# Kernel optimization log

Hardware: AMD Instinct MI355X
Metric: run time of the kernel (lower is better)

Reference implementation:

```python
import jax, jax.numpy as jnp
import numpy as np
from jax import lax

DIM = 256
HEADS = 8
EPS = 1e-12  # torch F.normalize default eps
DN = ('NCHW', 'OIHW', 'NCHW')


def conv1x1(x, w):
    return lax.conv_general_dilated(x, w, (1, 1), 'VALID', dimension_numbers=DN)


def dwconv3x3(x, w):
    c = x.shape[1]
    return lax.conv_general_dilated(x, w, (1, 1), ((1, 1), (1, 1)),
                                    dimension_numbers=DN, feature_group_count=c)


def setup_inputs() -> dict:
    key = jax.random.key(0)
    ks = jax.random.split(key, 8)
    B, C, H, W = 4, DIM, 160, 160
    s = lambda fan: 1.0 / np.sqrt(fan)
    return {
        'low': jax.random.normal(ks[0], (B, C, H, W), jnp.float32),
        'high': jax.random.normal(ks[1], (B, C, H, W), jnp.float32),
        'q_w': jax.random.normal(ks[2], (C, C, 1, 1), jnp.float32) * s(C),
        'q_dw_w': jax.random.normal(ks[3], (C, 1, 3, 3), jnp.float32) * s(9),
        'kv_w': jax.random.normal(ks[4], (2 * C, C, 1, 1), jnp.float32) * s(C),
        'kv_dw_w': jax.random.normal(ks[5], (2 * C, 1, 3, 3), jnp.float32) * s(9),
        'proj_w': jax.random.normal(ks[6], (C, C, 1, 1), jnp.float32) * s(C),
        'temperature': jnp.ones((HEADS, 1, 1), jnp.float32),
    }


def reference(low, high, q_w, q_dw_w, kv_w, kv_dw_w, proj_w, temperature):
    B, C, H, W = low.shape
    hw = H * W
    ch = C // HEADS  # channels per head

    q = dwconv3x3(conv1x1(high, q_w), q_dw_w)           # [B, C, H, W]
    kv = dwconv3x3(conv1x1(low, kv_w), kv_dw_w)         # [B, 2C, H, W]
    k, v = jnp.split(kv, 2, axis=1)

    def heads(x):
        return x.reshape(B, HEADS, ch, hw)              # b head c (h w)

    q, k, v = heads(q), heads(k), heads(v)

    # L2-normalize along spatial dim (torch F.normalize semantics)
    q = q / jnp.maximum(jnp.linalg.norm(q, axis=-1, keepdims=True), EPS)
    k = k / jnp.maximum(jnp.linalg.norm(k, axis=-1, keepdims=True), EPS)

    attn = jnp.einsum('bhcn,bhdn->bhcd', q, k) * temperature  # [B, H, ch, ch]
    attn = jax.nn.softmax(attn, axis=-1)
    out = jnp.einsum('bhcd,bhdn->bhcn', attn, v)               # [B, H, ch, hw]

    out = out.reshape(B, C, H, W)
    return conv1x1(out, proj_w)
```

## Files before the change

kernel.cpp:

```cpp
#include <hip/hip_runtime.h>
#include <math.h>

#define HW 25600
#define IMGW 160
#define CDIM 256
#define NB 4
#define NHEADS 8
#define SZB ((long)CDIM * HW)

typedef __attribute__((ext_vector_type(8))) short short8v;
typedef __attribute__((ext_vector_type(4))) float f32x4;
typedef __attribute__((ext_vector_type(8))) unsigned short us8;

union FragU {
    us8 o;
    short8v s;
    unsigned u32[4];
};

__device__ inline unsigned short f2bf(float f) {
    unsigned u = __float_as_uint(f);
    return (unsigned short)((u + 0x7fffu + ((u >> 16) & 1u)) >> 16);
}
__device__ inline float bf2f(unsigned short h) {
    return __uint_as_float(((unsigned)h) << 16);
}

__global__ __launch_bounds__(256) void cvtw_k(
    const float* __restrict__ kv_w, const float* __restrict__ q_w,
    unsigned short* __restrict__ wkv_s, unsigned short* __restrict__ wq_s)
{
    int idx = blockIdx.x * 256 + threadIdx.x;
    int g2 = idx & 3;
    int kt = (idx >> 2) & 7;
    int co = idx >> 5;
    const float* src;
    unsigned short* dst;
    int nco, co_l;
    if (co < 512) { src = kv_w; dst = wkv_s; nco = 512; co_l = co; }
    else          { src = q_w;  dst = wq_s;  nco = 256; co_l = co - 512; }
    src += (long)co_l * CDIM + kt * 32 + g2 * 8;
    us8 v;
#pragma unroll
    for (int u = 0; u < 8; ++u) v[u] = f2bf(src[u]);
    int slot = g2 ^ ((co_l >> 1) & 3);
    *(us8*)(dst + ((long)kt * nco + co_l) * 32 + slot * 8) = v;
}

template<int OUTF32, int XF32>
__global__ __launch_bounds__(256) void gemm3_k(
    const void* __restrict__ Xv, const unsigned short* __restrict__ WS,
    void* __restrict__ outp, long xbs, long wbs, long obs, int nco)
{
    __shared__ __align__(16) char SMEM[36864];
    unsigned short* Wl = (unsigned short*)SMEM;
    unsigned short* Xl = (unsigned short*)(SMEM + 16384);
    const int XST = XF32 ? 5120 : 4096;

    const int t  = threadIdx.x;
    const int l  = t & 63;
    const int wv = t >> 6;
    const int g  = l >> 4;
    const int ln = l & 15;

    const int NX = gridDim.x;
    const int orig = blockIdx.y * NX + blockIdx.x;
    const int chunkp = (NX * gridDim.y) >> 3;
    const int wgid = (orig & 7) * chunkp + (orig >> 3);
    const int co0 = (wgid % NX) * 128;
    const int n0  = (wgid / NX) * 128;

    const long b  = blockIdx.z;
    const unsigned short* Wb  = WS + b * wbs;
    const float* Xfp          = (const float*)Xv + b * xbs;
    const unsigned short* Xbf = (const unsigned short*)Xv + b * xbs;
    const int wr = wv >> 1, wc = wv & 1;

    f32x4 acc[4][4];
#pragma unroll
    for (int i = 0; i < 4; ++i)
#pragma unroll
        for (int j = 0; j < 4; ++j) acc[i][j] = (f32x4){0.f, 0.f, 0.f, 0.f};

    const int lrow = l >> 2;
    const int lgrp = l & 3;
    const int n_l = t & 127;
    const int sb  = (t >> 7) * 2;

    float f[16];

#define STAGE_W(ktv, buf)                                                     \
    {                                                                         \
        _Pragma("unroll")                                                     \
        for (int ii = 0; ii < 2; ++ii) {                                      \
            int instr = wv * 2 + ii;                                          \
            int row = instr * 16 + lrow;                                      \
            const unsigned short* wsrc =                                      \
                Wb + ((long)(ktv) * nco + co0 + row) * 32 + lgrp * 8;         \
            __builtin_amdgcn_global_load_lds(                                 \
                (const __attribute__((address_space(1))) void*)wsrc,          \
                (__attribute__((address_space(3))) void*)                     \
                    &Wl[(buf) * 4096 + instr * 512], 16, 0, 0);               \
        }                                                                     \
    }
#define STAGE_XG(ktv, buf)                                                    \
    {                                                                         \
        _Pragma("unroll")                                                     \
        for (int ii = 0; ii < 2; ++ii) {                                      \
            int instr = wv * 2 + ii;                                          \
            int row = instr * 16 + lrow;                                      \
            const unsigned short* xsrc =                                      \
                Xbf + ((long)(ktv) * HW + n0 + row) * 32 + lgrp * 8;          \
            __builtin_amdgcn_global_load_lds(                                 \
                (const __attribute__((address_space(1))) void*)xsrc,          \
                (__attribute__((address_space(3))) void*)                     \
                    &Xl[(buf) * 4096 + instr * 512], 16, 0, 0);               \
        }                                                                     \
    }
#define LOAD_XF(ktv)                                                          \
    {                                                                         \
        _Pragma("unroll")                                                     \
        for (int si = 0; si < 2; ++si)                                        \
            _Pragma("unroll")                                                 \
            for (int u = 0; u < 8; ++u)                                       \
                f[si * 8 + u] =                                               \
                    Xfp[(long)((ktv) * 32 + (sb + si) * 8 + u) * HW + n0 + n_l]; \
    }
#define WRITE_XF(buf)                                                         \
    {                                                                         \
        _Pragma("unroll")                                                     \
        for (int si = 0; si < 2; ++si) {                                      \
            FragU cv;                                                         \
            _Pragma("unroll")                                                 \
            for (int e2 = 0; e2 < 4; ++e2) {                                  \
                unsigned rr;                                                  \
                asm("v_cvt_pk_bf16_f32 %0, %1, %2"                            \
                    : "=v"(rr) : "v"(f[si * 8 + e2 * 2]),                     \
                      "v"(f[si * 8 + e2 * 2 + 1]));                           \
                cv.u32[e2] = rr;                                              \
            }                                                                 \
            *(us8*)&Xl[(buf) * XST + n_l * 40 + (sb + si) * 8] = cv.o;        \
        }                                                                     \
    }

    STAGE_W(0, 0);
    if (XF32) { LOAD_XF(0); WRITE_XF(0); }
    else      { STAGE_XG(0, 0); }
    __syncthreads();

    for (int kt = 0; kt < 8; ++kt) {
        const int cur = kt & 1, nxt = cur ^ 1;
        if (kt < 7) {
            STAGE_W(kt + 1, nxt);
            if (XF32) { LOAD_XF(kt + 1); }
            else      { STAGE_XG(kt + 1, nxt); }
        }
        FragU A_[4], B_[4];
#pragma unroll
        for (int i = 0; i < 4; ++i) {
            int row = wr * 64 + i * 16 + ln;
            int slot = g ^ ((row >> 1) & 3);
            A_[i].o = *(const us8*)&Wl[cur * 4096 + row * 32 + slot * 8];
        }
        if (XF32) {
#pragma unroll
            for (int j = 0; j < 4; ++j) {
                int row = wc * 64 + j * 16 + ln;
                B_[j].o = *(const us8*)&Xl[cur * XST + row * 40 + g * 8];
            }
        } else {
#pragma unroll
            for (int j = 0; j < 4; ++j) {
                int row = wc * 64 + j * 16 + ln;
                int slot = g ^ ((row >> 1) & 3);
                B_[j].o = *(const us8*)&Xl[cur * XST + row * 32 + slot * 8];
            }
        }
#pragma unroll
        for (int i = 0; i < 4; ++i)
#pragma unroll
            for (int j = 0; j < 4; ++j)
                acc[i][j] = __builtin_amdgcn_mfma_f32_16x16x32_bf16(
                    A_[i].s, B_[j].s, acc[i][j], 0, 0, 0);
        if (kt < 7 && XF32) { WRITE_XF(nxt); }
        __syncthreads();
    }
#undef STAGE_W
#undef STAGE_XG
#undef LOAD_XF
#undef WRITE_XF

    if (OUTF32) {
        float* ef = (float*)SMEM;
        float* ob = (float*)outp + b * obs;
#pragma unroll
        for (int h2 = 0; h2 < 2; ++h2) {
            if (wr == h2) {
#pragma unroll
                for (int i = 0; i < 4; ++i)
#pragma unroll
                    for (int j = 0; j < 4; ++j)
#pragma unroll
                        for (int r = 0; r < 4; ++r)
                            ef[(i * 16 + g * 4 + r) * 132 + wc * 64 + j * 16 + ln]
                                = acc[i][j][r];
            }
            __syncthreads();
#pragma unroll
            for (int p = 0; p < 8; ++p) {
                int idx = p * 256 + t;
                int row = idx >> 5;
                int c4 = (idx & 31) * 4;
                float4 v = *(const float4*)&ef[row * 132 + c4];
                *(float4*)(ob + (long)(co0 + h2 * 64 + row) * HW + n0 + c4) = v;
            }
            __syncthreads();
        }
    } else {
        unsigned short* eb = (unsigned short*)SMEM;
        unsigned short* ob = (unsigned short*)outp + b * obs;
#pragma unroll
        for (int i = 0; i < 4; ++i)
#pragma unroll
            for (int j = 0; j < 4; ++j)
#pragma unroll
                for (int r = 0; r < 4; ++r)
                    eb[(wr * 64 + i * 16 + g * 4 + r) * 136 + wc * 64 + j * 16 + ln]
                        = f2bf(acc[i][j][r]);
        __syncthreads();
#pragma unroll
        for (int p = 0; p < 8; ++p) {
            int idx = p * 256 + t;
            int row = idx >> 4;
            int c8 = (idx & 15) * 8;
            us8 v = *(const us8*)&eb[row * 136 + c8];
            *(us8*)(ob + (long)(co0 + row) * HW + n0 + c8) = v;
        }
    }
}

__global__ __launch_bounds__(256) void dwK_k(
    const unsigned short* __restrict__ A, const float* __restrict__ w,
    unsigned short* __restrict__ out, long bstride)
{
    __shared__ unsigned short xsh[8][10][168];
    const int t = threadIdx.x;
    const int y0 = blockIdx.x * 8;
    const int c0 = blockIdx.y * 8;
    const long b = blockIdx.z;
    const unsigned short* Ab = A + b * bstride;

    for (int idx = t; idx < 1600; idx += 256) {
        int seg = idx % 20;
        int row = (idx / 20) % 10;
        int ch  = idx / 200;
        int yy  = y0 + row - 1;
        us8 v = (us8){0, 0, 0, 0, 0, 0, 0, 0};
        if (yy >= 0 && yy < IMGW)
            v = *(const us8*)(Ab + (long)(c0 + ch) * HW + yy * IMGW + seg * 8);
        *(us8*)&xsh[ch][row][seg * 8] = v;
    }
    __syncthreads();

    const int ch = t >> 5;
    const int rem = t & 31;
    const int ro = rem >> 2;
    const int xq = rem & 3;
    float wreg[9];
#pragma unroll
    for (int u = 0; u < 9; ++u) wreg[u] = w[(c0 + ch) * 9 + u];
    unsigned short* ob = out + b * SZB + (long)(c0 + ch) * HW + (y0 + ro) * IMGW;

#pragma unroll
    for (int xs = 0; xs < 5; ++xs) {
        int x = xq * 8 + xs * 32;
        float s[8];
#pragma unroll
        for (int p = 0; p < 8; ++p) s[p] = 0.f;
#pragma unroll
        for (int dy = 0; dy < 3; ++dy) {
            const unsigned short* rp = &xsh[ch][ro + dy][0];
            float r[10];
            r[0] = (x > 0) ? bf2f(rp[x - 1]) : 0.f;
            us8 mid = *(const us8*)&rp[x];
#pragma unroll
            for (int u = 0; u < 8; ++u) r[1 + u] = bf2f(mid[u]);
            r[9] = (x + 8 < IMGW) ? bf2f(rp[x + 8]) : 0.f;
            float w0 = wreg[dy * 3], w1 = wreg[dy * 3 + 1], w2 = wreg[dy * 3 + 2];
#pragma unroll
            for (int p = 0; p < 8; ++p)
                s[p] = fmaf(w0, r[p], fmaf(w1, r[p + 1], fmaf(w2, r[p + 2], s[p])));
        }
        us8 o;
#pragma unroll
        for (int p = 0; p < 8; ++p) o[p] = f2bf(s[p]);
        *(us8*)(ob + x) = o;
    }
}

__global__ __launch_bounds__(256) void dwV_k(
    const unsigned short* __restrict__ A, const float* __restrict__ w,
    unsigned short* __restrict__ out, long bstride)
{
    __shared__ unsigned short xsh[16][6][168];
    __shared__ unsigned short osh[640][17];
    const int t = threadIdx.x;
    const int y0 = blockIdx.x * 4;
    const int c0 = blockIdx.y * 16;
    const long b = blockIdx.z;
    const unsigned short* Ab = A + b * bstride;

    for (int idx = t; idx < 1920; idx += 256) {
        int seg = idx % 20;
        int row = (idx / 20) % 6;
        int ch  = idx / 120;
        int yy  = y0 + row - 1;
        us8 v = (us8){0, 0, 0, 0, 0, 0, 0, 0};
        if (yy >= 0 && yy < IMGW)
            v = *(const us8*)(Ab + (long)(c0 + ch) * HW + yy * IMGW + seg * 8);
        *(us8*)&xsh[ch][row][seg * 8] = v;
    }
    __syncthreads();

    {
        const int ch = t >> 4;
        const int rem = t & 15;
        const int ro = rem >> 2;
        const int xq = rem & 3;
        float wreg[9];
#pragma unroll
        for (int u = 0; u < 9; ++u) wreg[u] = w[(c0 + ch) * 9 + u];
#pragma unroll
        for (int xs = 0; xs < 5; ++xs) {
            int x = xq * 8 + xs * 32;
            float s[8];
#pragma unroll
            for (int p = 0; p < 8; ++p) s[p] = 0.f;
#pragma unroll
            for (int dy = 0; dy < 3; ++dy) {
                const unsigned short* rp = &xsh[ch][ro + dy][0];
                float r[10];
                r[0] = (x > 0) ? bf2f(rp[x - 1]) : 0.f;
                us8 mid = *(const us8*)&rp[x];
#pragma unroll
                for (int u = 0; u < 8; ++u) r[1 + u] = bf2f(mid[u]);
                r[9] = (x + 8 < IMGW) ? bf2f(rp[x + 8]) : 0.f;
                float w0 = wreg[dy * 3], w1 = wreg[dy * 3 + 1], w2 = wreg[dy * 3 + 2];
#pragma unroll
                for (int p = 0; p < 8; ++p)
                    s[p] = fmaf(w0, r[p], fmaf(w1, r[p + 1], fmaf(w2, r[p + 2], s[p])));
            }
            int nl = ro * IMGW + x;
#pragma unroll
            for (int p = 0; p < 8; ++p) osh[nl + p][ch] = f2bf(s[p]);
        }
    }
    __syncthreads();

    for (int idx = t; idx < 1280; idx += 256) {
        int nl = idx >> 1;
        int c8 = (idx & 1) * 8;
        us8 o;
#pragma unroll
        for (int u = 0; u < 8; ++u) o[u] = osh[nl][c8 + u];
        int n  = y0 * IMGW + nl;
        int cg = c0 + c8;
        int kt = cg >> 5;
        int g2 = (cg >> 3) & 3;
        int slot = g2 ^ ((n >> 1) & 3);
        *(us8*)(out + b * SZB + ((long)kt * HW + n) * 32 + slot * 8) = o;
    }
}

__global__ __launch_bounds__(256) void gram_k(
    const unsigned short* __restrict__ q, const unsigned short* __restrict__ k,
    float* __restrict__ part_qk, float* __restrict__ part_sq_q,
    float* __restrict__ part_sq_k)
{
    __shared__ float Sred[4 * 1024];
    __shared__ float sqq_l[4][32];
    __shared__ float sqk_l[4][32];
    const int t  = threadIdx.x;
    const int l  = t & 63;
    const int wv = t >> 6;
    const int g  = l >> 4;
    const int ln = l & 15;
    const int chunk = blockIdx.x;
    const int h = blockIdx.y;
    const int b = blockIdx.z;

    f32x4 accS[2][2], accQ[2], accK[2];
#pragma unroll
    for (int i = 0; i < 2; ++i) {
        accQ[i] = (f32x4){0, 0, 0, 0};
        accK[i] = (f32x4){0, 0, 0, 0};
#pragma unroll
        for (int j = 0; j < 2; ++j) accS[i][j] = (f32x4){0, 0, 0, 0};
    }

    const unsigned short* qb = q + (long)b * SZB + (long)(h * 32) * HW;
    const unsigned short* kb = k + (long)b * SZB + (long)(h * 32) * HW;
    long nb = (long)chunk * 3200 + wv * 800;
    for (int s = 0; s < 25; ++s, nb += 32) {
        FragU aq[2], bk[2];
#pragma unroll
        for (int i = 0; i < 2; ++i)
            aq[i].o = *(const us8*)(qb + (long)(i * 16 + ln) * HW + nb + g * 8);
#pragma unroll
        for (int j = 0; j < 2; ++j)
            bk[j].o = *(const us8*)(kb + (long)(j * 16 + ln) * HW + nb + g * 8);
#pragma unroll
        for (int i = 0; i < 2; ++i)
#pragma unroll
            for (int j = 0; j < 2; ++j)
                accS[i][j] = __builtin_amdgcn_mfma_f32_16x16x32_bf16(
                    aq[i].s, bk[j].s, accS[i][j], 0, 0, 0);
#pragma unroll
        for (int i = 0; i < 2; ++i) {
            accQ[i] = __builtin_amdgcn_mfma_f32_16x16x32_bf16(
                aq[i].s, aq[i].s, accQ[i], 0, 0, 0);
            accK[i] = __builtin_amdgcn_mfma_f32_16x16x32_bf16(
                bk[i].s, bk[i].s, accK[i], 0, 0, 0);
        }
    }
#pragma unroll
    for (int i = 0; i < 2; ++i)
#pragma unroll
        for (int j = 0; j < 2; ++j)
#pragma unroll
            for (int r = 0; r < 4; ++r) {
                int row = i * 16 + g * 4 + r;
                int col = j * 16 + ln;
                Sred[wv * 1024 + row * 32 + col] = accS[i][j][r];
            }
#pragma unroll
    for (int i = 0; i < 2; ++i)
#pragma unroll
        for (int r = 0; r < 4; ++r)
            if (ln == g * 4 + r) {
                sqq_l[wv][i * 16 + g * 4 + r] = accQ[i][r];
                sqk_l[wv][i * 16 + g * 4 + r] = accK[i][r];
            }
    __syncthreads();
    const long pb = ((long)(b * NHEADS + h) * 8 + chunk);
#pragma unroll
    for (int e0 = 0; e0 < 4; ++e0) {
        int e = e0 * 256 + t;
        float v = Sred[e] + Sred[1024 + e] + Sred[2048 + e] + Sred[3072 + e];
        part_qk[pb * 1024 + e] = v;
    }
    if (t < 32)
        part_sq_q[pb * 32 + t] = sqq_l[0][t] + sqq_l[1][t] + sqq_l[2][t] + sqq_l[3][t];
    else if (t < 64) {
        int j = t - 32;
        part_sq_k[pb * 32 + j] = sqk_l[0][j] + sqk_l[1][j] + sqk_l[2][j] + sqk_l[3][j];
    }
}

__global__ __launch_bounds__(256) void attn_weff_k(
    const float* __restrict__ part_qk, const float* __restrict__ part_sq_q,
    const float* __restrict__ part_sq_k, const float* __restrict__ proj_w,
    const float* __restrict__ temp, unsigned short* __restrict__ weff_s)
{
    __shared__ float at[32 * 33];
    __shared__ float nq[32], nk[32];
    int bh = blockIdx.x;
    int b = bh >> 3, h = bh & 7;
    int t = threadIdx.x;
    long pb0 = (long)bh * 8;
    float4 s = make_float4(0, 0, 0, 0);
    for (int c = 0; c < 8; ++c) {
        float4 v = *(const float4*)(part_qk + (pb0 + c) * 1024 + t * 4);
        s.x += v.x; s.y += v.y; s.z += v.z; s.w += v.w;
    }
    if (t < 32) {
        float a = 0;
        for (int c = 0; c < 8; ++c) a += part_sq_q[(pb0 + c) * 32 + t];
        nq[t] = fmaxf(sqrtf(a), 1e-12f);
    } else if (t < 64) {
        int j = t - 32;
        float a = 0;
        for (int c = 0; c < 8; ++c) a += part_sq_k[(pb0 + c) * 32 + j];
        nk[j] = fmaxf(sqrtf(a), 1e-12f);
    }
    __syncthreads();
    float tp = temp[h];
    int ci = t >> 3, cj0 = (t & 7) * 4;
    at[ci * 33 + cj0 + 0] = s.x / (nq[ci] * nk[cj0 + 0]) * tp;
    at[ci * 33 + cj0 + 1] = s.y / (nq[ci] * nk[cj0 + 1]) * tp;
    at[ci * 33 + cj0 + 2] = s.z / (nq[ci] * nk[cj0 + 2]) * tp;
    at[ci * 33 + cj0 + 3] = s.w / (nq[ci] * nk[cj0 + 3]) * tp;
    __syncthreads();
    if (t < 32) {
        float m = -1e30f;
        for (int j = 0; j < 32; ++j) m = fmaxf(m, at[t * 33 + j]);
        float ss = 0;
        for (int j = 0; j < 32; ++j) {
            float e = expf(at[t * 33 + j] - m);
            at[t * 33 + j] = e;
            ss += e;
        }
        float inv = 1.f / ss;
        for (int j = 0; j < 32; ++j) at[t * 33 + j] *= inv;
    }
    __syncthreads();
    int co = t;
    float pw[32];
#pragma unroll
    for (int i2 = 0; i2 < 32; ++i2) pw[i2] = proj_w[(long)co * CDIM + h * 32 + i2];
    unsigned short* wb = weff_s + (long)b * 65536 + (long)h * (256 * 32) + co * 32;
    int swz = (co >> 1) & 3;
    for (int j = 0; j < 32; ++j) {
        float a = 0;
#pragma unroll
        for (int i2 = 0; i2 < 32; ++i2) a = fmaf(pw[i2], at[i2 * 33 + j], a);
        wb[((j >> 3) ^ swz) * 8 + (j & 7)] = f2bf(a);
    }
}

extern "C" void kernel_launch(void* const* d_in, const int* in_sizes, int n_in,
                              void* d_out, int out_size, void* d_ws, size_t ws_size,
                              hipStream_t stream)
{
    const float* low    = (const float*)d_in[0];
    const float* high   = (const float*)d_in[1];
    const float* q_w    = (const float*)d_in[2];
    const float* q_dw   = (const float*)d_in[3];
    const float* kv_w   = (const float*)d_in[4];
    const float* kv_dw  = (const float*)d_in[5];
    const float* proj_w = (const float*)d_in[6];
    const float* temp   = (const float*)d_in[7];
    float* out = (float*)d_out;

    unsigned short* usws = (unsigned short*)d_ws;
    unsigned short* Areg = usws;
    unsigned short* VT   = Areg + 8 * SZB;
    unsigned short* wkv_s = VT + 4 * SZB;
    unsigned short* wq_s  = wkv_s + 131072;
    unsigned short* weff_s = wq_s + 65536;
    float* part_qk   = (float*)(weff_s + 4L * 65536);
    float* part_sq_q = part_qk + 32L * 8 * 1024;
    float* part_sq_k = part_sq_q + 32L * 8 * 32;
    float* endp      = part_sq_k + 32L * 8 * 32;
    if (ws_size < (size_t)((char*)endp - (char*)d_ws)) return;

    unsigned short* K_all = (unsigned short*)d_out;
    unsigned short* Q_all = K_all + 4 * SZB;

    dim3 blk(256);

    cvtw_k<<<dim3(96), blk, 0, stream>>>(kv_w, q_w, wkv_s, wq_s);

    gemm3_k<0, 1><<<dim3(4, 200, NB), blk, 0, stream>>>(
        low, wkv_s, Areg, SZB, 0, 2 * SZB, 512);
    dwK_k<<<dim3(20, 32, NB), blk, 0, stream>>>(Areg, kv_dw, K_all, 2 * SZB);
    dwV_k<<<dim3(40, 16, NB), blk, 0, stream>>>(Areg + 256L * HW,
                                                kv_dw + 256 * 9, VT, 2 * SZB);

    gemm3_k<0, 1><<<dim3(2, 200, NB), blk, 0, stream>>>(
        high, wq_s, Areg, SZB, 0, 2 * SZB, 256);
    dwK_k<<<dim3(20, 32, NB), blk, 0, stream>>>(Areg, q_dw, Q_all, 2 * SZB);

    gram_k<<<dim3(8, NHEADS, NB), blk, 0, stream>>>(Q_all, K_all, part_qk,
                                                    part_sq_q, part_sq_k);
    attn_weff_k<<<dim3(32), blk, 0, stream>>>(
        part_qk, part_sq_q, part_sq_k, proj_w, temp, weff_s);

    gemm3_k<1, 0><<<dim3(2, 200, NB), blk, 0, stream>>>(VT, weff_s, out,
                                                        SZB, 65536, SZB, 256);
}
```

Measured before the change: 288.7 us.

## Triple-buffer GEMM LDS stages with prefetch depth two and manual waitcnts

Switches the 1x1-conv GEMM kernel from double to triple buffering in LDS, prefetching two k-tiles ahead. Explicit vmcnt/lgkmcnt waits and raw s_barrier replace the per-iteration __syncthreads so global loads stay in flight across iterations. This is meant to hide global memory latency. The cost is more LDS per block (up to 54KB), which may reduce occupancy, and more fragile hand-tuned wait counts.

```diff
diff --git a/kernel.cpp b/kernel.cpp
--- a/kernel.cpp
+++ b/kernel.cpp
@@ -48,14 +48,14 @@
 }
 
 template<int OUTF32, int XF32>
-__global__ __launch_bounds__(256) void gemm3_k(
+__global__ __launch_bounds__(256) void gemm4_k(
     const void* __restrict__ Xv, const unsigned short* __restrict__ WS,
     void* __restrict__ outp, long xbs, long wbs, long obs, int nco)
 {
-    __shared__ __align__(16) char SMEM[36864];
+    constexpr int XSTR = XF32 ? 5120 : 4096;
+    __shared__ __align__(16) char SMEM[XF32 ? 55296 : 49152];
     unsigned short* Wl = (unsigned short*)SMEM;
-    unsigned short* Xl = (unsigned short*)(SMEM + 16384);
-    const int XST = XF32 ? 5120 : 4096;
+    unsigned short* Xl = (unsigned short*)(SMEM + 24576);
 
     const int t  = threadIdx.x;
     const int l  = t & 63;
@@ -114,7 +114,7 @@
             __builtin_amdgcn_global_load_lds(                                 \
                 (const __attribute__((address_space(1))) void*)xsrc,          \
                 (__attribute__((address_space(3))) void*)                     \
-                    &Xl[(buf) * 4096 + instr * 512], 16, 0, 0);               \
+                    &Xl[(buf) * XSTR + instr * 512], 16, 0, 0);               \
         }                                                                     \
     }
 #define LOAD_XF(ktv)                                                          \
@@ -139,56 +139,88 @@
                       "v"(f[si * 8 + e2 * 2 + 1]));                           \
                 cv.u32[e2] = rr;                                              \
             }                                                                 \
-            *(us8*)&Xl[(buf) * XST + n_l * 40 + (sb + si) * 8] = cv.o;        \
+            *(us8*)&Xl[(buf) * XSTR + n_l * 40 + (sb + si) * 8] = cv.o;       \
         }                                                                     \
     }
 
-    STAGE_W(0, 0);
-    if (XF32) { LOAD_XF(0); WRITE_XF(0); }
-    else      { STAGE_XG(0, 0); }
-    __syncthreads();
-
-    for (int kt = 0; kt < 8; ++kt) {
-        const int cur = kt & 1, nxt = cur ^ 1;
-        if (kt < 7) {
-            STAGE_W(kt + 1, nxt);
-            if (XF32) { LOAD_XF(kt + 1); }
-            else      { STAGE_XG(kt + 1, nxt); }
+    if (XF32) {
+        LOAD_XF(0); STAGE_W(0, 0);
+        asm volatile("s_waitcnt vmcnt(2)" ::: "memory");
+        __builtin_amdgcn_sched_barrier(0);
+        WRITE_XF(0);
+        LOAD_XF(1); STAGE_W(1, 1);
+        asm volatile("s_waitcnt vmcnt(2)" ::: "memory");
+        __builtin_amdgcn_sched_barrier(0);
+        WRITE_XF(1);
+        asm volatile("s_waitcnt lgkmcnt(0)" ::: "memory");
+    } else {
+        STAGE_XG(0, 0); STAGE_W(0, 0);
+        STAGE_XG(1, 1); STAGE_W(1, 1);
+        asm volatile("s_waitcnt vmcnt(4)" ::: "memory");
+    }
+    __builtin_amdgcn_s_barrier();
+    __builtin_amdgcn_sched_barrier(0);
+
+#pragma unroll
+    for (int i = 0; i < 8; ++i) {
+        const int cb = i % 3;
+        const int nb2 = (i + 2) % 3;
+        if (i < 6) {
+            if (XF32) { LOAD_XF(i + 2); STAGE_W(i + 2, nb2); }
+            else      { STAGE_XG(i + 2, nb2); STAGE_W(i + 2, nb2); }
         }
         FragU A_[4], B_[4];
 #pragma unroll
-        for (int i = 0; i < 4; ++i) {
-            int row = wr * 64 + i * 16 + ln;
+        for (int ii = 0; ii < 4; ++ii) {
+            int row = wr * 64 + ii * 16 + ln;
             int slot = g ^ ((row >> 1) & 3);
-            A_[i].o = *(const us8*)&Wl[cur * 4096 + row * 32 + slot * 8];
+            A_[ii].o = *(const us8*)&Wl[cb * 4096 + row * 32 + slot * 8];
         }
         if (XF32) {
 #pragma unroll
             for (int j = 0; j < 4; ++j) {
                 int row = wc * 64 + j * 16 + ln;
-                B_[j].o = *(const us8*)&Xl[cur * XST + row * 40 + g * 8];
+                B_[j].o = *(const us8*)&Xl[cb * XSTR + row * 40 + g * 8];
             }
         } else {
 #pragma unroll
             for (int j = 0; j < 4; ++j) {
                 int row = wc * 64 + j * 16 + ln;
                 int slot = g ^ ((row >> 1) & 3);
-                B_[j].o = *(const us8*)&Xl[cur * XST + row * 32 + slot * 8];
-            }
-        }
-#pragma unroll
-        for (int i = 0; i < 4; ++i)
+                B_[j].o = *(const us8*)&Xl[cb * XSTR + row * 32 + slot * 8];
+            }
+        }
+#pragma unroll
+        for (int ii = 0; ii < 4; ++ii)
 #pragma unroll
             for (int j = 0; j < 4; ++j)
-                acc[i][j] = __builtin_amdgcn_mfma_f32_16x16x32_bf16(
-                    A_[i].s, B_[j].s, acc[i][j], 0, 0, 0);
-        if (kt < 7 && XF32) { WRITE_XF(nxt); }
-        __syncthreads();
+                acc[ii][j] = __builtin_amdgcn_mfma_f32_16x16x32_bf16(
+                    A_[ii].s, B_[j].s, acc[ii][j], 0, 0, 0);
+
+        if (i < 6) {
+            if (XF32) {
+                asm volatile("s_waitcnt vmcnt(2)" ::: "memory");
+                __builtin_amdgcn_sched_barrier(0);
+                WRITE_XF(nb2);
+                asm volatile("s_waitcnt lgkmcnt(0)" ::: "memory");
+            } else {
+                asm volatile("s_waitcnt vmcnt(4)" ::: "memory");
+                __builtin_amdgcn_sched_barrier(0);
+            }
+        } else {
+            asm volatile("s_waitcnt vmcnt(0)" ::: "memory");
+            __builtin_amdgcn_sched_barrier(0);
+        }
+        if (i < 7) {
+            __builtin_amdgcn_s_barrier();
+            __builtin_amdgcn_sched_barrier(0);
+        }
     }
 #undef STAGE_W
 #undef STAGE_XG
 #undef LOAD_XF
 #undef WRITE_XF
+    __syncthreads();
 
     if (OUTF32) {
         float* ef = (float*)SMEM;
@@ -551,13 +583,13 @@
 
     cvtw_k<<<dim3(96), blk, 0, stream>>>(kv_w, q_w, wkv_s, wq_s);
 
-    gemm3_k<0, 1><<<dim3(4, 200, NB), blk, 0, stream>>>(
+    gemm4_k<0, 1><<<dim3(4, 200, NB), blk, 0, stream>>>(
         low, wkv_s, Areg, SZB, 0, 2 * SZB, 512);
     dwK_k<<<dim3(20, 32, NB), blk, 0, stream>>>(Areg, kv_dw, K_all, 2 * SZB);
     dwV_k<<<dim3(40, 16, NB), blk, 0, stream>>>(Areg + 256L * HW,
                                                 kv_dw + 256 * 9, VT, 2 * SZB);
 
-    gemm3_k<0, 1><<<dim3(2, 200, NB), blk, 0, stream>>>(
+    gemm4_k<0, 1><<<dim3(2, 200, NB), blk, 0, stream>>>(
         high, wq_s, Areg, SZB, 0, 2 * SZB, 256);
     dwK_k<<<dim3(20, 32, NB), blk, 0, stream>>>(Areg, q_dw, Q_all, 2 * SZB);
 
@@ -566,6 +598,6 @@
     attn_weff_k<<<dim3(32), blk, 0, stream>>>(
         part_qk, part_sq_q, part_sq_k, proj_w, temp, weff_s);
 
-    gemm3_k<1, 0><<<dim3(2, 200, NB), blk, 0, stream>>>(VT, weff_s, out,
+    gemm4_k<1, 0><<<dim3(2, 200, NB), blk, 0, stream>>>(VT, weff_s, out,
                                                         SZB, 65536, SZB, 256);
 }
```

Measured after the change: 308.0 us. 6.7% more time.

## Pre-shuffle weights into MFMA fragment order and load them directly from global

Applied to the files above, without the earlier changes.

The weight matrices are now written by the conversion and attention kernels in the exact per-lane MFMA A-fragment order, so the GEMM reads A fragments straight from global memory (cache) and no longer stages W through LDS. This cuts LDS use per block, which may allow higher occupancy, and removes the W global-to-LDS copies. The epilogue is split into smaller chunks to fit the reduced shared buffer, and s_setprio is placed around the MFMA block. In exchange, the global weight loads now sit on the critical path of every k-step, and the extra epilogue barriers add synchronization.

```diff
diff --git a/kernel.cpp b/kernel.cpp
--- a/kernel.cpp
+++ b/kernel.cpp
@@ -28,34 +28,35 @@
 
 __global__ __launch_bounds__(256) void cvtw_k(
     const float* __restrict__ kv_w, const float* __restrict__ q_w,
-    unsigned short* __restrict__ wkv_s, unsigned short* __restrict__ wq_s)
+    unsigned short* __restrict__ wkvf, unsigned short* __restrict__ wqf)
 {
     int idx = blockIdx.x * 256 + threadIdx.x;
-    int g2 = idx & 3;
-    int kt = (idx >> 2) & 7;
-    int co = idx >> 5;
     const float* src;
     unsigned short* dst;
-    int nco, co_l;
-    if (co < 512) { src = kv_w; dst = wkv_s; nco = 512; co_l = co; }
-    else          { src = q_w;  dst = wq_s;  nco = 256; co_l = co - 512; }
-    src += (long)co_l * CDIM + kt * 32 + g2 * 8;
-    us8 v;
-#pragma unroll
-    for (int u = 0; u < 8; ++u) v[u] = f2bf(src[u]);
-    int slot = g2 ^ ((co_l >> 1) & 3);
-    *(us8*)(dst + ((long)kt * nco + co_l) * 32 + slot * 8) = v;
+    int rel;
+    if (idx < 16384) { src = kv_w; dst = wkvf; rel = idx; }
+    else             { src = q_w;  dst = wqf;  rel = idx - 16384; }
+    int l  = rel & 63;
+    int kt = (rel >> 6) & 7;
+    int c  = rel >> 9;
+    int co = c * 16 + (l & 15);
+    int k0 = kt * 32 + (l >> 4) * 8;
+    const float* s = src + (long)co * CDIM + k0;
+    us8 o;
+#pragma unroll
+    for (int u = 0; u < 8; ++u) o[u] = f2bf(s[u]);
+    *(us8*)(dst + (long)rel * 8) = o;
 }
 
 template<int OUTF32, int XF32>
-__global__ __launch_bounds__(256) void gemm3_k(
-    const void* __restrict__ Xv, const unsigned short* __restrict__ WS,
-    void* __restrict__ outp, long xbs, long wbs, long obs, int nco)
-{
-    __shared__ __align__(16) char SMEM[36864];
-    unsigned short* Wl = (unsigned short*)SMEM;
-    unsigned short* Xl = (unsigned short*)(SMEM + 16384);
-    const int XST = XF32 ? 5120 : 4096;
+__global__ __launch_bounds__(256) void gemm7_k(
+    const void* __restrict__ Xv, const unsigned short* __restrict__ Wf,
+    void* __restrict__ outp, long xbs, long wbs, long obs)
+{
+    constexpr int XBUFS = XF32 ? 5120 : 4096;
+    constexpr int SMEMB = XF32 ? 20480 : (OUTF32 ? 16896 : 16384);
+    __shared__ __align__(16) char SMEM[SMEMB];
+    unsigned short* Xl = (unsigned short*)SMEM;
 
     const int t  = threadIdx.x;
     const int l  = t & 63;
@@ -71,10 +72,11 @@
     const int n0  = (wgid / NX) * 128;
 
     const long b  = blockIdx.z;
-    const unsigned short* Wb  = WS + b * wbs;
+    const unsigned short* Wb  = Wf + b * wbs;
     const float* Xfp          = (const float*)Xv + b * xbs;
     const unsigned short* Xbf = (const unsigned short*)Xv + b * xbs;
     const int wr = wv >> 1, wc = wv & 1;
+    const int cbase = (co0 >> 4) + wr * 4;
 
     f32x4 acc[4][4];
 #pragma unroll
@@ -89,20 +91,6 @@
 
     float f[16];
 
-#define STAGE_W(ktv, buf)                                                     \
-    {                                                                         \
-        _Pragma("unroll")                                                     \
-        for (int ii = 0; ii < 2; ++ii) {                                      \
-            int instr = wv * 2 + ii;                                          \
-            int row = instr * 16 + lrow;                                      \
-            const unsigned short* wsrc =                                      \
-                Wb + ((long)(ktv) * nco + co0 + row) * 32 + lgrp * 8;         \
-            __builtin_amdgcn_global_load_lds(                                 \
-                (const __attribute__((address_space(1))) void*)wsrc,          \
-                (__attribute__((address_space(3))) void*)                     \
-                    &Wl[(buf) * 4096 + instr * 512], 16, 0, 0);               \
-        }                                                                     \
-    }
 #define STAGE_XG(ktv, buf)                                                    \
     {                                                                         \
         _Pragma("unroll")                                                     \
@@ -114,7 +102,7 @@
             __builtin_amdgcn_global_load_lds(                                 \
                 (const __attribute__((address_space(1))) void*)xsrc,          \
                 (__attribute__((address_space(3))) void*)                     \
-                    &Xl[(buf) * 4096 + instr * 512], 16, 0, 0);               \
+                    &Xl[(buf) * XBUFS + instr * 512], 16, 0, 0);              \
         }                                                                     \
     }
 #define LOAD_XF(ktv)                                                          \
@@ -139,53 +127,50 @@
                       "v"(f[si * 8 + e2 * 2 + 1]));                           \
                 cv.u32[e2] = rr;                                              \
             }                                                                 \
-            *(us8*)&Xl[(buf) * XST + n_l * 40 + (sb + si) * 8] = cv.o;        \
+            *(us8*)&Xl[(buf) * XBUFS + n_l * 40 + (sb + si) * 8] = cv.o;      \
         }                                                                     \
     }
 
-    STAGE_W(0, 0);
     if (XF32) { LOAD_XF(0); WRITE_XF(0); }
     else      { STAGE_XG(0, 0); }
     __syncthreads();
 
+#pragma unroll
     for (int kt = 0; kt < 8; ++kt) {
         const int cur = kt & 1, nxt = cur ^ 1;
         if (kt < 7) {
-            STAGE_W(kt + 1, nxt);
             if (XF32) { LOAD_XF(kt + 1); }
             else      { STAGE_XG(kt + 1, nxt); }
         }
         FragU A_[4], B_[4];
 #pragma unroll
-        for (int i = 0; i < 4; ++i) {
-            int row = wr * 64 + i * 16 + ln;
-            int slot = g ^ ((row >> 1) & 3);
-            A_[i].o = *(const us8*)&Wl[cur * 4096 + row * 32 + slot * 8];
-        }
+        for (int i = 0; i < 4; ++i)
+            A_[i].o = *(const us8*)&Wb[(((long)(cbase + i) * 8 + kt) * 64 + l) * 8];
         if (XF32) {
 #pragma unroll
             for (int j = 0; j < 4; ++j) {
                 int row = wc * 64 + j * 16 + ln;
-                B_[j].o = *(const us8*)&Xl[cur * XST + row * 40 + g * 8];
+                B_[j].o = *(const us8*)&Xl[cur * XBUFS + row * 40 + g * 8];
             }
         } else {
 #pragma unroll
             for (int j = 0; j < 4; ++j) {
                 int row = wc * 64 + j * 16 + ln;
                 int slot = g ^ ((row >> 1) & 3);
-                B_[j].o = *(const us8*)&Xl[cur * XST + row * 32 + slot * 8];
-            }
-        }
+                B_[j].o = *(const us8*)&Xl[cur * XBUFS + row * 32 + slot * 8];
+            }
+        }
+        __builtin_amdgcn_s_setprio(1);
 #pragma unroll
         for (int i = 0; i < 4; ++i)
 #pragma unroll
             for (int j = 0; j < 4; ++j)
                 acc[i][j] = __builtin_amdgcn_mfma_f32_16x16x32_bf16(
                     A_[i].s, B_[j].s, acc[i][j], 0, 0, 0);
+        __builtin_amdgcn_s_setprio(0);
         if (kt < 7 && XF32) { WRITE_XF(nxt); }
         __syncthreads();
     }
-#undef STAGE_W
 #undef STAGE_XG
 #undef LOAD_XF
 #undef WRITE_XF
@@ -194,25 +179,26 @@
         float* ef = (float*)SMEM;
         float* ob = (float*)outp + b * obs;
 #pragma unroll
-        for (int h2 = 0; h2 < 2; ++h2) {
-            if (wr == h2) {
-#pragma unroll
-                for (int i = 0; i < 4; ++i)
+        for (int p = 0; p < 4; ++p) {
+            if (wr == (p >> 1)) {
+                int ib = (p & 1) * 2;
+#pragma unroll
+                for (int i2 = 0; i2 < 2; ++i2)
 #pragma unroll
                     for (int j = 0; j < 4; ++j)
 #pragma unroll
                         for (int r = 0; r < 4; ++r)
-                            ef[(i * 16 + g * 4 + r) * 132 + wc * 64 + j * 16 + ln]
-                                = acc[i][j][r];
+                            ef[(i2 * 16 + g * 4 + r) * 132 + wc * 64 + j * 16 + ln]
+                                = acc[ib + i2][j][r];
             }
             __syncthreads();
 #pragma unroll
-            for (int p = 0; p < 8; ++p) {
-                int idx = p * 256 + t;
+            for (int pp = 0; pp < 4; ++pp) {
+                int idx = pp * 256 + t;
                 int row = idx >> 5;
                 int c4 = (idx & 31) * 4;
                 float4 v = *(const float4*)&ef[row * 132 + c4];
-                *(float4*)(ob + (long)(co0 + h2 * 64 + row) * HW + n0 + c4) = v;
+                *(float4*)(ob + (long)(co0 + p * 32 + row) * HW + n0 + c4) = v;
             }
             __syncthreads();
         }
@@ -220,21 +206,27 @@
         unsigned short* eb = (unsigned short*)SMEM;
         unsigned short* ob = (unsigned short*)outp + b * obs;
 #pragma unroll
-        for (int i = 0; i < 4; ++i)
-#pragma unroll
-            for (int j = 0; j < 4; ++j)
-#pragma unroll
-                for (int r = 0; r < 4; ++r)
-                    eb[(wr * 64 + i * 16 + g * 4 + r) * 136 + wc * 64 + j * 16 + ln]
-                        = f2bf(acc[i][j][r]);
-        __syncthreads();
-#pragma unroll
-        for (int p = 0; p < 8; ++p) {
-            int idx = p * 256 + t;
-            int row = idx >> 4;
-            int c8 = (idx & 15) * 8;
-            us8 v = *(const us8*)&eb[row * 136 + c8];
-            *(us8*)(ob + (long)(co0 + row) * HW + n0 + c8) = v;
+        for (int p = 0; p < 2; ++p) {
+            if (wr == p) {
+#pragma unroll
+                for (int i = 0; i < 4; ++i)
+#pragma unroll
+                    for (int j = 0; j < 4; ++j)
+#pragma unroll
+                        for (int r = 0; r < 4; ++r)
+                            eb[(i * 16 + g * 4 + r) * 136 + wc * 64 + j * 16 + ln]
+                                = f2bf(acc[i][j][r]);
+            }
+            __syncthreads();
+#pragma unroll
+            for (int pp = 0; pp < 4; ++pp) {
+                int idx = pp * 256 + t;
+                int row = idx >> 4;
+                int c8 = (idx & 15) * 8;
+                us8 v = *(const us8*)&eb[row * 136 + c8];
+                *(us8*)(ob + (long)(co0 + p * 64 + row) * HW + n0 + c8) = v;
+            }
+            __syncthreads();
         }
     }
 }
@@ -460,7 +452,7 @@
 __global__ __launch_bounds__(256) void attn_weff_k(
     const float* __restrict__ part_qk, const float* __restrict__ part_sq_q,
     const float* __restrict__ part_sq_k, const float* __restrict__ proj_w,
-    const float* __restrict__ temp, unsigned short* __restrict__ weff_s)
+    const float* __restrict__ temp, unsigned short* __restrict__ wefff)
 {
     __shared__ float at[32 * 33];
     __shared__ float nq[32], nk[32];
@@ -508,13 +500,15 @@
     float pw[32];
 #pragma unroll
     for (int i2 = 0; i2 < 32; ++i2) pw[i2] = proj_w[(long)co * CDIM + h * 32 + i2];
-    unsigned short* wb = weff_s + (long)b * 65536 + (long)h * (256 * 32) + co * 32;
-    int swz = (co >> 1) & 3;
+    unsigned short* wb = wefff + (long)b * 65536;
+    int chi = co >> 4, lr = co & 15;
     for (int j = 0; j < 32; ++j) {
         float a = 0;
 #pragma unroll
         for (int i2 = 0; i2 < 32; ++i2) a = fmaf(pw[i2], at[i2 * 33 + j], a);
-        wb[((j >> 3) ^ swz) * 8 + (j & 7)] = f2bf(a);
+        int g2 = j >> 3, e = j & 7;
+        long idx = ((long)(chi * 8 + h) * 64 + g2 * 16 + lr) * 8 + e;
+        wb[idx] = f2bf(a);
     }
 }
 
@@ -535,10 +529,10 @@
     unsigned short* usws = (unsigned short*)d_ws;
     unsigned short* Areg = usws;
     unsigned short* VT   = Areg + 8 * SZB;
-    unsigned short* wkv_s = VT + 4 * SZB;
-    unsigned short* wq_s  = wkv_s + 131072;
-    unsigned short* weff_s = wq_s + 65536;
-    float* part_qk   = (float*)(weff_s + 4L * 65536);
+    unsigned short* wkvf = VT + 4 * SZB;
+    unsigned short* wqf  = wkvf + 131072;
+    unsigned short* wefff = wqf + 65536;
+    float* part_qk   = (float*)(wefff + 4L * 65536);
     float* part_sq_q = part_qk + 32L * 8 * 1024;
     float* part_sq_k = part_sq_q + 32L * 8 * 32;
     float* endp      = part_sq_k + 32L * 8 * 32;
@@ -549,23 +543,23 @@
 
     dim3 blk(256);
 
-    cvtw_k<<<dim3(96), blk, 0, stream>>>(kv_w, q_w, wkv_s, wq_s);
-
-    gemm3_k<0, 1><<<dim3(4, 200, NB), blk, 0, stream>>>(
-        low, wkv_s, Areg, SZB, 0, 2 * SZB, 512);
+    cvtw_k<<<dim3(96), blk, 0, stream>>>(kv_w, q_w, wkvf, wqf);
+
+    gemm7_k<0, 1><<<dim3(4, 200, NB), blk, 0, stream>>>(
+        low, wkvf, Areg, SZB, 0, 2 * SZB);
     dwK_k<<<dim3(20, 32, NB), blk, 0, stream>>>(Areg, kv_dw, K_all, 2 * SZB);
     dwV_k<<<dim3(40, 16, NB), blk, 0, stream>>>(Areg + 256L * HW,
                                                 kv_dw + 256 * 9, VT, 2 * SZB);
 
-    gemm3_k<0, 1><<<dim3(2, 200, NB), blk, 0, stream>>>(
-        high, wq_s, Areg, SZB, 0, 2 * SZB, 256);
+    gemm7_k<0, 1><<<dim3(2, 200, NB), blk, 0, stream>>>(
+        high, wqf, Areg, SZB, 0, 2 * SZB);
     dwK_k<<<dim3(20, 32, NB), blk, 0, stream>>>(Areg, q_dw, Q_all, 2 * SZB);
 
     gram_k<<<dim3(8, NHEADS, NB), blk, 0, stream>>>(Q_all, K_all, part_qk,
                                                     part_sq_q, part_sq_k);
     attn_weff_k<<<dim3(32), blk, 0, stream>>>(
-        part_qk, part_sq_q, part_sq_k, proj_w, temp, weff_s);
-
-    gemm3_k<1, 0><<<dim3(2, 200, NB), blk, 0, stream>>>(VT, weff_s, out,
-                                                        SZB, 65536, SZB, 256);
-}
+        part_qk, part_sq_q, part_sq_k, proj_w, temp, wefff);
+
+    gemm7_k<1, 0><<<dim3(2, 200, NB), blk, 0, stream>>>(
+        VT, wefff, out, SZB, 65536, SZB);
+}
```

New measurement: 318.8 us. +10.4%, slower.

## Enlarge GEMM tile to 256x128 with 512-thread blocks for 1x1 convs

Applied to the files above, without the earlier changes.

The 1x1-conv GEMM kernel now uses 512-thread workgroups (8 waves) covering 256 output channels by 128 pixels instead of 128x128. Each X tile is staged once for twice as many output channels, so the fp32 activation input is read and converted to bf16 fewer times. Weight staging buffers double, and the epilogue writes its output through shared memory in more synchronized passes. The grids are halved to match, which lowers the number of workgroups and may reduce occupancy or load balance.

```diff
diff --git a/kernel.cpp b/kernel.cpp
--- a/kernel.cpp
+++ b/kernel.cpp
@@ -48,14 +48,15 @@
 }
 
 template<int OUTF32, int XF32>
-__global__ __launch_bounds__(256) void gemm3_k(
+__global__ __launch_bounds__(512, 4) void gemm8_k(
     const void* __restrict__ Xv, const unsigned short* __restrict__ WS,
     void* __restrict__ outp, long xbs, long wbs, long obs, int nco)
 {
-    __shared__ __align__(16) char SMEM[36864];
+    constexpr int XBUFS = XF32 ? 5120 : 4096;
+    constexpr int WBUFS = 8192;
+    __shared__ __align__(16) char SMEM[32768 + 2 * XBUFS * 2];
     unsigned short* Wl = (unsigned short*)SMEM;
-    unsigned short* Xl = (unsigned short*)(SMEM + 16384);
-    const int XST = XF32 ? 5120 : 4096;
+    unsigned short* Xl = (unsigned short*)(SMEM + 32768);
 
     const int t  = threadIdx.x;
     const int l  = t & 63;
@@ -67,7 +68,7 @@
     const int orig = blockIdx.y * NX + blockIdx.x;
     const int chunkp = (NX * gridDim.y) >> 3;
     const int wgid = (orig & 7) * chunkp + (orig >> 3);
-    const int co0 = (wgid % NX) * 128;
+    const int co0 = (wgid % NX) * 256;
     const int n0  = (wgid / NX) * 128;
 
     const long b  = blockIdx.z;
@@ -85,9 +86,9 @@
     const int lrow = l >> 2;
     const int lgrp = l & 3;
     const int n_l = t & 127;
-    const int sb  = (t >> 7) * 2;
-
-    float f[16];
+    const int sb8 = (t >> 7) * 8;
+
+    float f[8];
 
 #define STAGE_W(ktv, buf)                                                     \
     {                                                                         \
@@ -100,47 +101,36 @@
             __builtin_amdgcn_global_load_lds(                                 \
                 (const __attribute__((address_space(1))) void*)wsrc,          \
                 (__attribute__((address_space(3))) void*)                     \
-                    &Wl[(buf) * 4096 + instr * 512], 16, 0, 0);               \
+                    &Wl[(buf) * WBUFS + instr * 512], 16, 0, 0);              \
         }                                                                     \
     }
 #define STAGE_XG(ktv, buf)                                                    \
     {                                                                         \
-        _Pragma("unroll")                                                     \
-        for (int ii = 0; ii < 2; ++ii) {                                      \
-            int instr = wv * 2 + ii;                                          \
-            int row = instr * 16 + lrow;                                      \
-            const unsigned short* xsrc =                                      \
-                Xbf + ((long)(ktv) * HW + n0 + row) * 32 + lgrp * 8;          \
-            __builtin_amdgcn_global_load_lds(                                 \
-                (const __attribute__((address_space(1))) void*)xsrc,          \
-                (__attribute__((address_space(3))) void*)                     \
-                    &Xl[(buf) * 4096 + instr * 512], 16, 0, 0);               \
-        }                                                                     \
+        int row = wv * 16 + lrow;                                             \
+        const unsigned short* xsrc =                                          \
+            Xbf + ((long)(ktv) * HW + n0 + row) * 32 + lgrp * 8;              \
+        __builtin_amdgcn_global_load_lds(                                     \
+            (const __attribute__((address_space(1))) void*)xsrc,              \
+            (__attribute__((address_space(3))) void*)                         \
+                &Xl[(buf) * XBUFS + wv * 512], 16, 0, 0);                     \
     }
 #define LOAD_XF(ktv)                                                          \
     {                                                                         \
         _Pragma("unroll")                                                     \
-        for (int si = 0; si < 2; ++si)                                        \
-            _Pragma("unroll")                                                 \
-            for (int u = 0; u < 8; ++u)                                       \
-                f[si * 8 + u] =                                               \
-                    Xfp[(long)((ktv) * 32 + (sb + si) * 8 + u) * HW + n0 + n_l]; \
+        for (int u = 0; u < 8; ++u)                                           \
+            f[u] = Xfp[(long)((ktv) * 32 + sb8 + u) * HW + n0 + n_l];         \
     }
 #define WRITE_XF(buf)                                                         \
     {                                                                         \
+        FragU cv;                                                             \
         _Pragma("unroll")                                                     \
-        for (int si = 0; si < 2; ++si) {                                      \
-            FragU cv;                                                         \
-            _Pragma("unroll")                                                 \
-            for (int e2 = 0; e2 < 4; ++e2) {                                  \
-                unsigned rr;                                                  \
-                asm("v_cvt_pk_bf16_f32 %0, %1, %2"                            \
-                    : "=v"(rr) : "v"(f[si * 8 + e2 * 2]),                     \
-                      "v"(f[si * 8 + e2 * 2 + 1]));                           \
-                cv.u32[e2] = rr;                                              \
-            }                                                                 \
-            *(us8*)&Xl[(buf) * XST + n_l * 40 + (sb + si) * 8] = cv.o;        \
+        for (int e2 = 0; e2 < 4; ++e2) {                                      \
+            unsigned rr;                                                      \
+            asm("v_cvt_pk_bf16_f32 %0, %1, %2"                                \
+                : "=v"(rr) : "v"(f[e2 * 2]), "v"(f[e2 * 2 + 1]));             \
+            cv.u32[e2] = rr;                                                  \
         }                                                                     \
+        *(us8*)&Xl[(buf) * XBUFS + n_l * 40 + sb8] = cv.o;                    \
     }
 
     STAGE_W(0, 0);
@@ -160,20 +150,20 @@
         for (int i = 0; i < 4; ++i) {
             int row = wr * 64 + i * 16 + ln;
             int slot = g ^ ((row >> 1) & 3);
-            A_[i].o = *(const us8*)&Wl[cur * 4096 + row * 32 + slot * 8];
+            A_[i].o = *(const us8*)&Wl[cur * WBUFS + row * 32 + slot * 8];
         }
         if (XF32) {
 #pragma unroll
             for (int j = 0; j < 4; ++j) {
                 int row = wc * 64 + j * 16 + ln;
-                B_[j].o = *(const us8*)&Xl[cur * XST + row * 40 + g * 8];
+                B_[j].o = *(const us8*)&Xl[cur * XBUFS + row * 40 + g * 8];
             }
         } else {
 #pragma unroll
             for (int j = 0; j < 4; ++j) {
                 int row = wc * 64 + j * 16 + ln;
                 int slot = g ^ ((row >> 1) & 3);
-                B_[j].o = *(const us8*)&Xl[cur * XST + row * 32 + slot * 8];
+                B_[j].o = *(const us8*)&Xl[cur * XBUFS + row * 32 + slot * 8];
             }
         }
 #pragma unroll
@@ -194,25 +184,26 @@
         float* ef = (float*)SMEM;
         float* ob = (float*)outp + b * obs;
 #pragma unroll
-        for (int h2 = 0; h2 < 2; ++h2) {
-            if (wr == h2) {
-#pragma unroll
-                for (int i = 0; i < 4; ++i)
+        for (int p = 0; p < 8; ++p) {
+            if (wr == (p >> 1)) {
+                int ib = (p & 1) * 2;
+#pragma unroll
+                for (int i2 = 0; i2 < 2; ++i2)
 #pragma unroll
                     for (int j = 0; j < 4; ++j)
 #pragma unroll
                         for (int r = 0; r < 4; ++r)
-                            ef[(i * 16 + g * 4 + r) * 132 + wc * 64 + j * 16 + ln]
-                                = acc[i][j][r];
+                            ef[(i2 * 16 + g * 4 + r) * 132 + wc * 64 + j * 16 + ln]
+                                = acc[ib + i2][j][r];
             }
             __syncthreads();
 #pragma unroll
-            for (int p = 0; p < 8; ++p) {
-                int idx = p * 256 + t;
+            for (int pp = 0; pp < 2; ++pp) {
+                int idx = pp * 512 + t;
                 int row = idx >> 5;
                 int c4 = (idx & 31) * 4;
                 float4 v = *(const float4*)&ef[row * 132 + c4];
-                *(float4*)(ob + (long)(co0 + h2 * 64 + row) * HW + n0 + c4) = v;
+                *(float4*)(ob + (long)(co0 + p * 32 + row) * HW + n0 + c4) = v;
             }
             __syncthreads();
         }
@@ -220,21 +211,27 @@
         unsigned short* eb = (unsigned short*)SMEM;
         unsigned short* ob = (unsigned short*)outp + b * obs;
 #pragma unroll
-        for (int i = 0; i < 4; ++i)
-#pragma unroll
-            for (int j = 0; j < 4; ++j)
-#pragma unroll
-                for (int r = 0; r < 4; ++r)
-                    eb[(wr * 64 + i * 16 + g * 4 + r) * 136 + wc * 64 + j * 16 + ln]
-                        = f2bf(acc[i][j][r]);
-        __syncthreads();
-#pragma unroll
-        for (int p = 0; p < 8; ++p) {
-            int idx = p * 256 + t;
-            int row = idx >> 4;
-            int c8 = (idx & 15) * 8;
-            us8 v = *(const us8*)&eb[row * 136 + c8];
-            *(us8*)(ob + (long)(co0 + row) * HW + n0 + c8) = v;
+        for (int p = 0; p < 4; ++p) {
+            if (wr == p) {
+#pragma unroll
+                for (int i = 0; i < 4; ++i)
+#pragma unroll
+                    for (int j = 0; j < 4; ++j)
+#pragma unroll
+                        for (int r = 0; r < 4; ++r)
+                            eb[(i * 16 + g * 4 + r) * 136 + wc * 64 + j * 16 + ln]
+                                = f2bf(acc[i][j][r]);
+            }
+            __syncthreads();
+#pragma unroll
+            for (int pp = 0; pp < 2; ++pp) {
+                int idx = pp * 512 + t;
+                int row = idx >> 4;
+                int c8 = (idx & 15) * 8;
+                us8 v = *(const us8*)&eb[row * 136 + c8];
+                *(us8*)(ob + (long)(co0 + p * 64 + row) * HW + n0 + c8) = v;
+            }
+            __syncthreads();
         }
     }
 }
@@ -548,16 +545,17 @@
     unsigned short* Q_all = K_all + 4 * SZB;
 
     dim3 blk(256);
+    dim3 blk512(512);
 
     cvtw_k<<<dim3(96), blk, 0, stream>>>(kv_w, q_w, wkv_s, wq_s);
 
-    gemm3_k<0, 1><<<dim3(4, 200, NB), blk, 0, stream>>>(
+    gemm8_k<0, 1><<<dim3(2, 200, NB), blk512, 0, stream>>>(
         low, wkv_s, Areg, SZB, 0, 2 * SZB, 512);
     dwK_k<<<dim3(20, 32, NB), blk, 0, stream>>>(Areg, kv_dw, K_all, 2 * SZB);
     dwV_k<<<dim3(40, 16, NB), blk, 0, stream>>>(Areg + 256L * HW,
                                                 kv_dw + 256 * 9, VT, 2 * SZB);
 
-    gemm3_k<0, 1><<<dim3(2, 200, NB), blk, 0, stream>>>(
+    gemm8_k<0, 1><<<dim3(1, 200, NB), blk512, 0, stream>>>(
         high, wq_s, Areg, SZB, 0, 2 * SZB, 256);
     dwK_k<<<dim3(20, 32, NB), blk, 0, stream>>>(Areg, q_dw, Q_all, 2 * SZB);
 
@@ -566,6 +564,6 @@
     attn_weff_k<<<dim3(32), blk, 0, stream>>>(
         part_qk, part_sq_q, part_sq_k, proj_w, temp, weff_s);
 
-    gemm3_k<1, 0><<<dim3(2, 200, NB), blk, 0, stream>>>(VT, weff_s, out,
-                                                        SZB, 65536, SZB, 256);
-}
+    gemm8_k<1, 0><<<dim3(1, 200, NB), blk512, 0, stream>>>(
+        VT, weff_s, out, SZB, 65536, SZB, 256);
+}
```

New measurement: 298.7 us. 3.5% more time.
